# Optimization experiments

Measured on AMD Instinct MI355X. Metric: run time of the kernel, lower is better.

Reference implementation:

```python
import jax, jax.numpy as jnp
import numpy as np

LMAX = 3
L2 = (LMAX + 1) ** 2
EPS = 1e-5
N_NODES = 2048
C_IN = 384
C_HID = 256


def _gaunt_tensor(lmax):
    # Real Gaunt coefficients G[i,j,k] = integral Y_i Y_j Y_k dOmega over S^2,
    # computed exactly with Gauss-Legendre (theta) x uniform (phi) quadrature.
    nt = 4 * lmax + 4
    nph = 8 * lmax + 8
    xg, wg = np.polynomial.legendre.leggauss(nt)
    ct, st = xg, np.sqrt(1.0 - xg ** 2)
    phi = 2.0 * np.pi * np.arange(nph) / nph
    # fully-normalized associated Legendre Pbar[l,m] on theta nodes
    P = np.zeros((lmax + 1, lmax + 1, nt))
    P[0, 0] = np.sqrt(1.0 / (4.0 * np.pi))
    for m in range(1, lmax + 1):
        P[m, m] = np.sqrt((2.0 * m + 1.0) / (2.0 * m)) * st * P[m - 1, m - 1]
    for m in range(lmax + 1):
        if m + 1 <= lmax:
            P[m + 1, m] = np.sqrt(2.0 * m + 3.0) * ct * P[m, m]
        for l in range(m + 2, lmax + 1):
            a = np.sqrt((4.0 * l * l - 1.0) / (l * l - m * m))
            b = np.sqrt(((l - 1.0) ** 2 - m * m) / (4.0 * (l - 1.0) ** 2 - 1.0))
            P[l, m] = a * (ct * P[l - 1, m] - b * P[l - 2, m])
    Y = np.zeros(((lmax + 1) ** 2, nt, nph))
    for l in range(lmax + 1):
        for m in range(-l, l + 1):
            idx = l * l + l + m
            if m == 0:
                Y[idx] = P[l, 0][:, None] * np.ones((1, nph))
            elif m > 0:
                Y[idx] = np.sqrt(2.0) * P[l, m][:, None] * np.cos(m * phi)[None, :]
            else:
                Y[idx] = np.sqrt(2.0) * P[l, -m][:, None] * np.sin(-m * phi)[None, :]
    W = wg[:, None] * (2.0 * np.pi / nph)  # [nt, nph]
    G = np.einsum('iap,jap,kap->ijk', Y, Y, Y * W[None])
    G[np.abs(G) < 1e-10] = 0.0
    return G


G_NP = _gaunt_tensor(LMAX)
SL = [slice(l * l, (l + 1) * (l + 1)) for l in range(LMAX + 1)]
_raw = []
for _l1 in range(LMAX + 1):
    for _l2 in range(LMAX + 1):
        for _l3 in range(LMAX + 1):
            _blk = G_NP[SL[_l1], SL[_l2], SL[_l3]]
            if np.abs(_blk).max() > 1e-8:
                _raw.append((_l1, _l2, _l3, _blk))
_fanin = {}
for _l1, _l2, _l3, _b in _raw:
    _fanin[_l3] = _fanin.get(_l3, 0) + 1
# component irrep normalization (sqrt(2l3+1)) and path normalization (1/sqrt(fan-in))
PATHS = [(l1, l2, l3, jnp.asarray((blk * np.sqrt(2.0 * l3 + 1.0) / np.sqrt(_fanin[l3])).astype(np.float32)))
         for (l1, l2, l3, blk) in _raw]
L_OF = jnp.asarray(np.repeat(np.arange(LMAX + 1), 2 * np.arange(LMAX + 1) + 1))  # [L2]


def setup_inputs() -> dict:
    key = jax.random.key(0)
    ks = jax.random.split(key, 9)
    inputs = jax.random.normal(ks[0], (N_NODES, L2, C_IN), jnp.float32)
    batch = jnp.sort(jax.random.randint(ks[1], (N_NODES,), 0, 64))
    norm_w = 1.0 + 0.1 * jax.random.normal(ks[2], (LMAX + 1, C_IN), jnp.float32)
    norm_b = 0.02 * jax.random.normal(ks[3], (C_IN,), jnp.float32)
    w1 = jax.random.normal(ks[4], (LMAX + 1, C_IN, C_HID), jnp.float32) / np.sqrt(C_IN)
    b1 = 0.02 * jax.random.normal(ks[5], (C_HID,), jnp.float32)
    w_gaunt = jax.random.normal(ks[6], (LMAX + 1, LMAX + 1, LMAX + 1, C_HID), jnp.float32)
    w2 = jax.random.normal(ks[7], (LMAX + 1, C_HID, C_IN), jnp.float32) / np.sqrt(C_HID)
    b2 = 0.02 * jax.random.normal(ks[8], (C_IN,), jnp.float32)
    return {"inputs": inputs, "batch": batch, "norm_w": norm_w, "norm_b": norm_b,
            "w1": w1, "b1": b1, "w_gaunt": w_gaunt, "w2": w2, "b2": b2}


def _forward(inputs, norm_w, norm_b, w1, b1, w_gaunt, w2, b2):
    # equivariant merge layer norm: center l=0 over channels, RMS over all (lm, C),
    # per-degree affine weight, bias on the l=0 (invariant) component only
    x = inputs
    x = x.at[:, 0, :].add(-jnp.mean(x[:, 0, :], axis=-1, keepdims=True))
    x = x * jax.lax.rsqrt(jnp.mean(x * x, axis=(1, 2), keepdims=True) + EPS)
    x = x * norm_w[L_OF][None]          # [N, L2, C]
    x = x.at[:, 0, :].add(norm_b)
    # SO3Linear 1: per-degree channel mixing, bias on l=0
    h = jnp.einsum('nic,ich->nih', x, w1[L_OF])
    h = h.at[:, 0, :].add(b1)
    # Gaunt depthwise self tensor product: per-channel CG-structured contraction
    t = jnp.zeros((inputs.shape[0], L2, w1.shape[-1]), dtype=h.dtype)
    for (l1, l2, l3, blk) in PATHS:
        hw = h[:, SL[l2], :] * w_gaunt[l1, l2, l3][None, None, :]     # [N, 2l2+1, H]
        tmp = jnp.einsum('ijk,nih->njkh', blk, h[:, SL[l1], :])       # small block contraction
        t = t.at[:, SL[l3], :].add(jnp.einsum('njkh,njh->nkh', tmp, hw))
    # SO3Linear 2
    out = jnp.einsum('nih,iho->nio', t, w2[L_OF])
    out = out.at[:, 0, :].add(b2)
    return out + inputs  # ffn_shortcut is Identity (num_in == num_out)


def reference(inputs, batch, norm_w, norm_b, w1, b1, w_gaunt, w2, b2):
    # drop_path / proj_drop are disabled (rates = 0); `batch` only feeds GraphDropPath
    return _forward(inputs, norm_w, norm_b, w1, b1, w_gaunt, w2, b2)
```

## Files before the change

kernel.cpp:

```cpp
#include <hip/hip_runtime.h>
#include <stdint.h>
#include <math.h>
#include <array>
#include <utility>

#ifndef M_PI
#define M_PI 3.14159265358979323846
#endif

#define NNODES 2048
#define L2DIM  16
#define CIN    384
#define CHID   256

typedef __attribute__((ext_vector_type(8))) short short8;
typedef __attribute__((ext_vector_type(4))) float f32x4;
typedef unsigned short u16;
typedef unsigned int   u32;

#define LOF(i) ((i) < 1 ? 0 : ((i) < 4 ? 1 : ((i) < 9 ? 2 : 3)))

static __device__ __forceinline__ u16 f2bf(float f) {
  u32 u = __builtin_bit_cast(u32, f);
  u = u + 0x7FFFu + ((u >> 16) & 1u);
  return (u16)(u >> 16);
}
static __device__ __forceinline__ float bf2f(u16 b) {
  u32 u = ((u32)b) << 16;
  return __builtin_bit_cast(float, u);
}

constexpr double CPI = 3.14159265358979323846;

constexpr double csqrt(double x) {
  if (x <= 0.0) return 0.0;
  double y = x > 1.0 ? x : 1.0;
  for (int i = 0; i < 48; ++i) y = 0.5 * (y + x / y);
  return y;
}
constexpr double ccos(double x) {
  double r = x;
  while (r > CPI)  r -= 2.0 * CPI;
  while (r < -CPI) r += 2.0 * CPI;
  double r2 = r * r, term = 1.0, sum = 1.0;
  for (int i = 1; i <= 26; ++i) { term *= -r2 / ((2.0 * i - 1.0) * (2.0 * i)); sum += term; }
  return sum;
}
constexpr int iabs_c(int x) { return x < 0 ? -x : x; }

struct GLQ { double x[16]; double w[16]; };
constexpr GLQ build_gl() {
  GLQ g{};
  const int n = 16;
  for (int i = 0; i < n; ++i) {
    double x = ccos(CPI * (i + 0.75) / (n + 0.5));
    double p1 = 0.0, dp = 1.0;
    for (int it = 0; it < 40; ++it) {
      double p0 = 1.0; p1 = x;
      for (int k = 2; k <= n; ++k) { double p2 = ((2.0*k-1.0)*x*p1 - (k-1.0)*p0)/k; p0 = p1; p1 = p2; }
      dp = n * (x*p1 - p0) / (x*x - 1.0);
      x -= p1 / dp;
    }
    { double p0 = 1.0; p1 = x;
      for (int k = 2; k <= n; ++k) { double p2 = ((2.0*k-1.0)*x*p1 - (k-1.0)*p0)/k; p0 = p1; p1 = p2; }
      dp = n * (x*p1 - p0) / (x*x - 1.0); }
    g.x[i] = x;
    g.w[i] = 2.0 / ((1.0 - x*x) * dp * dp);
  }
  return g;
}
constexpr GLQ QG = build_gl();

struct PTab { double v[4][4][16]; };
constexpr PTab build_pbar() {
  PTab T{};
  for (int t = 0; t < 16; ++t) {
    double ct = QG.x[t];
    double st = csqrt(1.0 - ct * ct);
    double P[4][4] = {};
    P[0][0] = csqrt(1.0 / (4.0 * CPI));
    for (int m = 1; m <= 3; ++m)
      P[m][m] = csqrt((2.0*m + 1.0) / (2.0*m)) * st * P[m-1][m-1];
    for (int m = 0; m <= 3; ++m) {
      if (m + 1 <= 3) P[m+1][m] = csqrt(2.0*m + 3.0) * ct * P[m][m];
      for (int l = m + 2; l <= 3; ++l) {
        double aa = csqrt((4.0*(double)l*l - 1.0) / ((double)l*l - (double)m*m));
        double bb = csqrt(((double)(l-1)*(l-1) - (double)m*m) / (4.0*(double)(l-1)*(l-1) - 1.0));
        P[l][m] = aa * (ct * P[l-1][m] - bb * P[l-2][m]);
      }
    }
    for (int l = 0; l < 4; ++l)
      for (int m = 0; m <= l; ++m) T.v[l][m][t] = P[l][m];
  }
  return T;
}
constexpr PTab PT = build_pbar();

constexpr double phi_int(int m1, int m2, int m3) {
  const double SQ2 = 1.41421356237309504880;
  int neg = (m1 < 0) + (m2 < 0) + (m3 < 0);
  if (neg & 1) return 0.0;
  int a = iabs_c(m1), b = iabs_c(m2), c = iabs_c(m3);
  int nz = (a > 0) + (b > 0) + (c > 0);
  if (nz == 0) return 2.0 * CPI;
  if (nz == 1) return 0.0;
  if (nz == 2) {
    int p = 0, q = 0;
    if (a == 0) { p = b; q = c; } else if (b == 0) { p = a; q = c; } else { p = a; q = b; }
    return (p == q) ? 2.0 * CPI : 0.0;
  }
  if (neg == 0) {
    double v = 0.0;
    if (iabs_c(a - b) == c && a != b) v += 1.0;
    if (a + b == c) v += 1.0;
    return SQ2 * CPI * v;
  }
  int p = 0, q = 0, r = 0;
  if (m1 > 0)      { p = a; q = b; r = c; }
  else if (m2 > 0) { p = b; q = a; r = c; }
  else             { p = c; q = a; r = b; }
  double v = 0.0;
  if (q != r && p == iabs_c(q - r)) v += 1.0;
  if (p == q + r) v -= 1.0;
  return SQ2 * CPI * v;
}

constexpr bool path_ok(int l1, int l2, int l3) {
  int lo = l1 > l2 ? l1 - l2 : l2 - l1;
  return l3 >= lo && l3 <= l1 + l2 && (((l1 + l2 + l3) & 1) == 0);
}
constexpr bool term_ok(int m1, int m2, int m3) {
  int aa = iabs_c(m1), bb = iabs_c(m2), cc = iabs_c(m3);
  int neg = (m1 < 0) + (m2 < 0) + (m3 < 0);
  if (neg & 1) return false;
  return (aa + bb == cc) || (bb + cc == aa) || (cc + aa == bb);
}
constexpr int count_paths() {
  int n = 0;
  for (int l1 = 0; l1 < 4; ++l1) for (int l2 = 0; l2 < 4; ++l2) for (int l3 = 0; l3 < 4; ++l3)
    if (path_ok(l1, l2, l3)) ++n;
  return n;
}
constexpr int NPATHS = count_paths();
constexpr int NTMAX  = 512;

constexpr double term_g(int l1, int m1, int l2, int m2, int l3, int m3) {
  double ph = phi_int(m1, m2, m3);
  if (ph == 0.0) return 0.0;
  int a = iabs_c(m1), b = iabs_c(m2), c = iabs_c(m3);
  double s = 0.0;
  for (int t = 0; t < 16; ++t)
    s += QG.w[t] * PT.v[l1][a][t] * PT.v[l2][b][t] * PT.v[l3][c][t];
  double g = ph * s;
  double fan = (l3 == 0) ? 4.0 : (l3 == 1 ? 6.0 : (l3 == 2 ? 7.0 : 6.0));
  return g * csqrt((2.0 * (double)l3 + 1.0) / fan);
}

struct TermG { float g; unsigned char i, j, k, p; };
struct PathT { unsigned char l1, l2, l3; };
struct TGAll { TermG t[NTMAX]; int n; };
constexpr TGAll build_all() {
  TGAll r{};
  r.n = 0;
  int p = 0;
  for (int l1 = 0; l1 < 4; ++l1) for (int l2 = 0; l2 < 4; ++l2) for (int l3 = 0; l3 < 4; ++l3) {
    if (!path_ok(l1, l2, l3)) continue;
    for (int m1 = -l1; m1 <= l1; ++m1) for (int m2 = -l2; m2 <= l2; ++m2) for (int m3 = -l3; m3 <= l3; ++m3) {
      if (!term_ok(m1, m2, m3)) continue;
      double g = term_g(l1, m1, l2, m2, l3, m3);
      if (g > 1e-10 || g < -1e-10) {
        r.t[r.n].g = (float)g;
        r.t[r.n].i = (unsigned char)(l1 * l1 + l1 + m1);
        r.t[r.n].j = (unsigned char)(l2 * l2 + l2 + m2);
        r.t[r.n].k = (unsigned char)(l3 * l3 + l3 + m3);
        r.t[r.n].p = (unsigned char)p;
        ++r.n;
      }
    }
    ++p;
  }
  return r;
}
constexpr TGAll TGA = build_all();
constexpr int NNZ = TGA.n;

constexpr std::array<PathT, NPATHS> build_paths() {
  std::array<PathT, NPATHS> a{};
  int n = 0;
  for (int l1 = 0; l1 < 4; ++l1) for (int l2 = 0; l2 < 4; ++l2) for (int l3 = 0; l3 < 4; ++l3)
    if (path_ok(l1, l2, l3)) a[n++] = PathT{(unsigned char)l1, (unsigned char)l2, (unsigned char)l3};
  return a;
}
constexpr auto PATHS_ARR = build_paths();

template <size_t... Is>
__device__ __forceinline__ void gaunt_terms(std::index_sequence<Is...>,
    float* __restrict__ t, const float* __restrict__ h,
    const float* __restrict__ wgv) {
  ((t[TGA.t[Is].k] = fmaf(TGA.t[Is].g * wgv[TGA.t[Is].p],
                          h[TGA.t[Is].i] * h[TGA.t[Is].j],
                          t[TGA.t[Is].k])), ...);
}
template <size_t... Ps>
__device__ __forceinline__ void load_wgv2(std::index_sequence<Ps...>,
    float* __restrict__ w0, float* __restrict__ w1,
    const float* __restrict__ wg, int c) {
  float2 tmp;
  (((tmp = *reinterpret_cast<const float2*>(
        &wg[(size_t)(((int)PATHS_ARR[Ps].l1 * 4 + (int)PATHS_ARR[Ps].l2) * 4
                     + (int)PATHS_ARR[Ps].l3) * CHID + c]),
     w0[Ps] = tmp.x, w1[Ps] = tmp.y)), ...);
}

__global__ __launch_bounds__(256) void prep_kernel(
    const float* __restrict__ x, const float* __restrict__ nw,
    const float* __restrict__ nb, u16* __restrict__ xnb,
    const float* __restrict__ w1, const float* __restrict__ w2,
    u16* __restrict__ w1t, u16* __restrict__ w2t) {
  int bid = blockIdx.x, tid = threadIdx.x;
  if (bid >= NNODES) {
    __shared__ float tile[32][33];
    int b2 = bid - NNODES;
    int z = b2 / 144, rem = b2 % 144;
    int by = rem / 12, bx = rem % 12;
    int R = z < 4 ? 384 : 256, C = z < 4 ? 256 : 384;
    int r0 = by * 32, c0 = bx * 32;
    if (r0 >= R || c0 >= C) return;
    const float* s = (z < 4 ? w1 : w2) + (size_t)(z & 3) * R * C;
    u16* d = (z < 4 ? w1t : w2t) + (size_t)(z & 3) * R * C;
    int tx = tid & 31, ty = tid >> 5;
    for (int rr = ty; rr < 32; rr += 8)
      tile[rr][tx] = s[(size_t)(r0 + rr) * C + (c0 + tx)];
    __syncthreads();
    for (int cc = ty; cc < 32; cc += 8)
      d[(size_t)(c0 + cc) * R + (r0 + tx)] = f2bf(tile[tx][cc]);
    return;
  }
  int n = bid;
  const float* xr = x + (size_t)n * (L2DIM * CIN);
  __shared__ float2 red[4];
  float4 v[6];
  float ssq = 0.f, m0p = 0.f;
#pragma unroll
  for (int q = 0; q < 6; ++q) {
    v[q] = reinterpret_cast<const float4*>(xr)[tid * 6 + q];
    ssq += v[q].x*v[q].x + v[q].y*v[q].y + v[q].z*v[q].z + v[q].w*v[q].w;
  }
  if (tid < 16) {
#pragma unroll
    for (int q = 0; q < 6; ++q) m0p += v[q].x + v[q].y + v[q].z + v[q].w;
  }
  float a = m0p, b = ssq;
#pragma unroll
  for (int off = 32; off > 0; off >>= 1) { a += __shfl_down(a, off, 64); b += __shfl_down(b, off, 64); }
  int lane = tid & 63, wid = tid >> 6;
  if (lane == 0) red[wid] = make_float2(a, b);
  __syncthreads();
  float sum0 = red[0].x + red[1].x + red[2].x + red[3].x;
  float ssqt = red[0].y + red[1].y + red[2].y + red[3].y;
  float mean0 = sum0 * (1.0f / CIN);
  float ss = ssqt - (float)CIN * mean0 * mean0;
  float rstd = rsqrtf(ss * (1.0f / (L2DIM * CIN)) + 1e-5f);

  int lm = tid >> 4;
  int l = LOF(lm);
  bool row0 = (lm == 0);
  int cbase = (tid & 15) * 24;
  u16* orow = xnb + (size_t)n * (L2DIM * CIN) + (size_t)tid * 24;
#pragma unroll
  for (int q = 0; q < 6; ++q) {
    int c = cbase + q * 4;
    float4 w4 = *reinterpret_cast<const float4*>(&nw[l * CIN + c]);
    float4 b4 = row0 ? *reinterpret_cast<const float4*>(&nb[c]) : make_float4(0,0,0,0);
    float sub = row0 ? mean0 : 0.f;
    float o0 = (v[q].x - sub) * rstd * w4.x + b4.x;
    float o1 = (v[q].y - sub) * rstd * w4.y + b4.y;
    float o2 = (v[q].z - sub) * rstd * w4.z + b4.z;
    float o3 = (v[q].w - sub) * rstd * w4.w + b4.w;
    ushort4 pk;
    pk.x = f2bf(o0); pk.y = f2bf(o1); pk.z = f2bf(o2); pk.w = f2bf(o3);
    *reinterpret_cast<ushort4*>(&orow[q * 4]) = pk;
  }
}

template <int KD, int ND, int BN, bool SECOND>
__global__ __launch_bounds__(512) void so3_gemm_kernel(
    const u16* __restrict__ A, const u16* __restrict__ BT,
    const float* __restrict__ bias, const float* __restrict__ resid,
    u16* __restrict__ outb, float* __restrict__ outf) {
  constexpr int NFRAG = BN / 64;
  constexpr int WN_T = BN / 4;
  constexpr int KT = KD / 64;
  static_assert((BN % 64) == 0 && NFRAG * 16 == WN_T, "");

  int l = blockIdx.z;
  int twol1 = 2 * l + 1;
  int mtiles = (NNODES * twol1) >> 6;
  if ((int)blockIdx.x >= mtiles) return;
  int col0 = blockIdx.y * BN;
  int tid = threadIdx.x, lane = tid & 63, wid = tid >> 6;
  int wm = wid >> 2, wn = wid & 3;

  __shared__ u16 Asm[2][64 * 64];
  __shared__ u16 Bsm[2][BN * 64];

  int ar = tid >> 3;
  const u16* asrc;
  {
    int Rg = blockIdx.x * 64 + ar;
    int node = Rg / twol1;
    int lm = l * l + (Rg - node * twol1);
    asrc = A + (size_t)(node * L2DIM + lm) * KD + ((tid & 7) ^ (ar & 7)) * 8;
  }
  const u16* bsrc[BN / 64];
#pragma unroll
  for (int i = 0; i < BN / 64; ++i) {
    int r = i * 64 + (tid >> 3);
    bsrc[i] = BT + (size_t)(l * ND + col0 + r) * KD + ((tid & 7) ^ (r & 7)) * 8;
  }

  auto stage = [&](int buf, int kt) {
    __builtin_amdgcn_global_load_lds(
        (const __attribute__((address_space(1))) void*)(asrc + kt * 64),
        (__attribute__((address_space(3))) void*)(&Asm[buf][wid * 512]),
        16, 0, 0);
#pragma unroll
    for (int i = 0; i < BN / 64; ++i)
      __builtin_amdgcn_global_load_lds(
          (const __attribute__((address_space(1))) void*)(bsrc[i] + kt * 64),
          (__attribute__((address_space(3))) void*)(&Bsm[buf][i * 4096 + wid * 512]),
          16, 0, 0);
  };

  f32x4 acc[2][NFRAG];
#pragma unroll
  for (int i = 0; i < 2; ++i)
#pragma unroll
    for (int j = 0; j < NFRAG; ++j) acc[i][j] = (f32x4){0.f, 0.f, 0.f, 0.f};

  stage(0, 0);
  __syncthreads();
#pragma unroll
  for (int kt = 0; kt < KT; ++kt) {
    int cur = kt & 1;
    if (kt + 1 < KT) stage(cur ^ 1, kt + 1);
#pragma unroll
    for (int ks = 0; ks < 2; ++ks) {
      short8 af[2], bfv[NFRAG];
#pragma unroll
      for (int mf = 0; mf < 2; ++mf) {
        int row = wm * 32 + mf * 16 + (lane & 15);
        int slot = (ks * 4 + (lane >> 4)) ^ (row & 7);
        af[mf] = *reinterpret_cast<const short8*>(&Asm[cur][row * 64 + slot * 8]);
      }
#pragma unroll
      for (int nf = 0; nf < NFRAG; ++nf) {
        int brow = wn * WN_T + nf * 16 + (lane & 15);
        int slot = (ks * 4 + (lane >> 4)) ^ (brow & 7);
        bfv[nf] = *reinterpret_cast<const short8*>(&Bsm[cur][brow * 64 + slot * 8]);
      }
#pragma unroll
      for (int mf = 0; mf < 2; ++mf)
#pragma unroll
        for (int nf = 0; nf < NFRAG; ++nf)
          acc[mf][nf] = __builtin_amdgcn_mfma_f32_16x16x32_bf16(af[mf], bfv[nf], acc[mf][nf], 0, 0, 0);
    }
    __syncthreads();
  }

#pragma unroll
  for (int mf = 0; mf < 2; ++mf) {
#pragma unroll
    for (int jj = 0; jj < 4; ++jj) {
      int Rg = blockIdx.x * 64 + wm * 32 + mf * 16 + (lane >> 4) * 4 + jj;
      int node = Rg / twol1;
      int lm = l * l + (Rg - node * twol1);
      size_t rowoff = (size_t)(node * L2DIM + lm);
#pragma unroll
      for (int nf = 0; nf < NFRAG; ++nf) {
        int colg = col0 + wn * WN_T + nf * 16 + (lane & 15);
        float vv = acc[mf][nf][jj];
        if (l == 0) vv += bias[colg];
        if (!SECOND) {
          outb[rowoff * ND + colg] = f2bf(vv);
        } else {
          outf[rowoff * ND + colg] = vv + resid[rowoff * ND + colg];
        }
      }
    }
  }
}

__global__ __launch_bounds__(256) void gaunt_kernel(
    const u16* __restrict__ hb, const float* __restrict__ wg,
    u16* __restrict__ tb) {
  int tid = threadIdx.x;
  int n = blockIdx.x * 2 + (tid >> 7);
  int c = (tid & 127) * 2;
  const u16* hr = hb + (size_t)n * (L2DIM * CHID) + c;
  float h0[16], h1[16];
#pragma unroll
  for (int i = 0; i < 16; ++i) {
    u32 w = *reinterpret_cast<const u32*>(&hr[i * CHID]);
    h0[i] = bf2f((u16)(w & 0xffffu));
    h1[i] = bf2f((u16)(w >> 16));
  }

  float w0[NPATHS], w1[NPATHS];
  load_wgv2(std::make_index_sequence<NPATHS>{}, w0, w1, wg, c);

  float t0[16], t1[16];
#pragma unroll
  for (int k = 0; k < 16; ++k) { t0[k] = 0.f; t1[k] = 0.f; }

  gaunt_terms(std::make_index_sequence<NNZ>{}, t0, h0, w0);
  gaunt_terms(std::make_index_sequence<NNZ>{}, t1, h1, w1);

  u16* tr = tb + (size_t)n * (L2DIM * CHID) + c;
#pragma unroll
  for (int k = 0; k < 16; ++k) {
    u32 o = (u32)f2bf(t0[k]) | ((u32)f2bf(t1[k]) << 16);
    *reinterpret_cast<u32*>(&tr[k * CHID]) = o;
  }
}

extern "C" void kernel_launch(void* const* d_in, const int* in_sizes, int n_in,
                              void* d_out, int out_size, void* d_ws, size_t ws_size,
                              hipStream_t stream) {
  const float* inputs = (const float*)d_in[0];
  const float* norm_w = (const float*)d_in[2];
  const float* norm_b = (const float*)d_in[3];
  const float* w1     = (const float*)d_in[4];
  const float* b1     = (const float*)d_in[5];
  const float* wga    = (const float*)d_in[6];
  const float* w2     = (const float*)d_in[7];
  const float* b2     = (const float*)d_in[8];
  float* out = (float*)d_out;

  uint8_t* ws = (uint8_t*)d_ws;
  u16*   w1t = (u16*)(ws + 16384);
  u16*   w2t = (u16*)(ws + 802816);
  u16*   xnb = (u16*)(ws + 1589248);
  u16*   tb  = xnb;
  u16*   hb  = (u16*)(ws + 26755072);

  prep_kernel<<<NNODES + 1152, 256, 0, stream>>>(
      inputs, norm_w, norm_b, xnb, w1, w2, w1t, w2t);
  so3_gemm_kernel<CIN, CHID, 128, false><<<dim3(224, 2, 4), 512, 0, stream>>>(
      xnb, w1t, b1, nullptr, hb, nullptr);
  gaunt_kernel<<<NNODES / 2, 256, 0, stream>>>(hb, wga, tb);
  so3_gemm_kernel<CHID, CIN, 128, true><<<dim3(224, 3, 4), 512, 0, stream>>>(
      tb, w2t, b2, inputs, nullptr, out);
}
```

Baseline: 83.60 us.

## Swap GEMM operand roles so each lane writes contiguous channel vectors

The SO3 linear GEMMs are recast in transposed form. Weights now fill the MFMA A side with 64 channels per block, and node rows fill the B side with 128 rows per block. In the epilogue each lane then holds four consecutive output channels, so bias, residual and output can be moved with vectorized float4/ushort4 accesses instead of scalar strided stores. The grid shape changes to match the new 128x64 tile, which changes how much of each operand is reused per block and the total block count.

```diff
diff --git a/kernel.cpp b/kernel.cpp
--- a/kernel.cpp
+++ b/kernel.cpp
@@ -283,60 +283,53 @@
   }
 }
 
-template <int KD, int ND, int BN, bool SECOND>
+template <int KD, int NDC, bool SECOND>
 __global__ __launch_bounds__(512) void so3_gemm_kernel(
-    const u16* __restrict__ A, const u16* __restrict__ BT,
+    const u16* __restrict__ X, const u16* __restrict__ WT,
     const float* __restrict__ bias, const float* __restrict__ resid,
     u16* __restrict__ outb, float* __restrict__ outf) {
-  constexpr int NFRAG = BN / 64;
-  constexpr int WN_T = BN / 4;
   constexpr int KT = KD / 64;
-  static_assert((BN % 64) == 0 && NFRAG * 16 == WN_T, "");
-
   int l = blockIdx.z;
   int twol1 = 2 * l + 1;
-  int mtiles = (NNODES * twol1) >> 6;
-  if ((int)blockIdx.x >= mtiles) return;
-  int col0 = blockIdx.y * BN;
+  if ((int)blockIdx.x >= 16 * twol1) return;
+  int bx = blockIdx.x, by = blockIdx.y;
   int tid = threadIdx.x, lane = tid & 63, wid = tid >> 6;
   int wm = wid >> 2, wn = wid & 3;
 
-  __shared__ u16 Asm[2][64 * 64];
-  __shared__ u16 Bsm[2][BN * 64];
-
-  int ar = tid >> 3;
-  const u16* asrc;
-  {
-    int Rg = blockIdx.x * 64 + ar;
+  __shared__ u16 Wsm[2][64 * 64];
+  __shared__ u16 Xsm[2][128 * 64];
+
+  int wr = tid >> 3;
+  const u16* wsrc = WT + (size_t)(l * NDC + by * 64 + wr) * KD
+                       + ((tid & 7) ^ (wr & 7)) * 8;
+  const u16* xsrc[2];
+#pragma unroll
+  for (int i = 0; i < 2; ++i) {
+    int xr = i * 64 + (tid >> 3);
+    int Rg = bx * 128 + xr;
     int node = Rg / twol1;
     int lm = l * l + (Rg - node * twol1);
-    asrc = A + (size_t)(node * L2DIM + lm) * KD + ((tid & 7) ^ (ar & 7)) * 8;
-  }
-  const u16* bsrc[BN / 64];
-#pragma unroll
-  for (int i = 0; i < BN / 64; ++i) {
-    int r = i * 64 + (tid >> 3);
-    bsrc[i] = BT + (size_t)(l * ND + col0 + r) * KD + ((tid & 7) ^ (r & 7)) * 8;
+    xsrc[i] = X + (size_t)(node * L2DIM + lm) * KD + ((tid & 7) ^ (xr & 7)) * 8;
   }
 
   auto stage = [&](int buf, int kt) {
     __builtin_amdgcn_global_load_lds(
-        (const __attribute__((address_space(1))) void*)(asrc + kt * 64),
-        (__attribute__((address_space(3))) void*)(&Asm[buf][wid * 512]),
+        (const __attribute__((address_space(1))) void*)(wsrc + kt * 64),
+        (__attribute__((address_space(3))) void*)(&Wsm[buf][wid * 512]),
         16, 0, 0);
 #pragma unroll
-    for (int i = 0; i < BN / 64; ++i)
+    for (int i = 0; i < 2; ++i)
       __builtin_amdgcn_global_load_lds(
-          (const __attribute__((address_space(1))) void*)(bsrc[i] + kt * 64),
-          (__attribute__((address_space(3))) void*)(&Bsm[buf][i * 4096 + wid * 512]),
+          (const __attribute__((address_space(1))) void*)(xsrc[i] + kt * 64),
+          (__attribute__((address_space(3))) void*)(&Xsm[buf][i * 4096 + wid * 512]),
           16, 0, 0);
   };
 
-  f32x4 acc[2][NFRAG];
+  f32x4 acc[2][2];
 #pragma unroll
   for (int i = 0; i < 2; ++i)
 #pragma unroll
-    for (int j = 0; j < NFRAG; ++j) acc[i][j] = (f32x4){0.f, 0.f, 0.f, 0.f};
+    for (int j = 0; j < 2; ++j) acc[i][j] = (f32x4){0.f, 0.f, 0.f, 0.f};
 
   stage(0, 0);
   __syncthreads();
@@ -346,24 +339,24 @@
     if (kt + 1 < KT) stage(cur ^ 1, kt + 1);
 #pragma unroll
     for (int ks = 0; ks < 2; ++ks) {
-      short8 af[2], bfv[NFRAG];
+      short8 wf[2], xf[2];
 #pragma unroll
       for (int mf = 0; mf < 2; ++mf) {
         int row = wm * 32 + mf * 16 + (lane & 15);
         int slot = (ks * 4 + (lane >> 4)) ^ (row & 7);
-        af[mf] = *reinterpret_cast<const short8*>(&Asm[cur][row * 64 + slot * 8]);
-      }
-#pragma unroll
-      for (int nf = 0; nf < NFRAG; ++nf) {
-        int brow = wn * WN_T + nf * 16 + (lane & 15);
-        int slot = (ks * 4 + (lane >> 4)) ^ (brow & 7);
-        bfv[nf] = *reinterpret_cast<const short8*>(&Bsm[cur][brow * 64 + slot * 8]);
+        wf[mf] = *reinterpret_cast<const short8*>(&Wsm[cur][row * 64 + slot * 8]);
+      }
+#pragma unroll
+      for (int nf = 0; nf < 2; ++nf) {
+        int row = wn * 32 + nf * 16 + (lane & 15);
+        int slot = (ks * 4 + (lane >> 4)) ^ (row & 7);
+        xf[nf] = *reinterpret_cast<const short8*>(&Xsm[cur][row * 64 + slot * 8]);
       }
 #pragma unroll
       for (int mf = 0; mf < 2; ++mf)
 #pragma unroll
-        for (int nf = 0; nf < NFRAG; ++nf)
-          acc[mf][nf] = __builtin_amdgcn_mfma_f32_16x16x32_bf16(af[mf], bfv[nf], acc[mf][nf], 0, 0, 0);
+        for (int nf = 0; nf < 2; ++nf)
+          acc[mf][nf] = __builtin_amdgcn_mfma_f32_16x16x32_bf16(wf[mf], xf[nf], acc[mf][nf], 0, 0, 0);
     }
     __syncthreads();
   }
@@ -371,21 +364,26 @@
 #pragma unroll
   for (int mf = 0; mf < 2; ++mf) {
 #pragma unroll
-    for (int jj = 0; jj < 4; ++jj) {
-      int Rg = blockIdx.x * 64 + wm * 32 + mf * 16 + (lane >> 4) * 4 + jj;
-      int node = Rg / twol1;
-      int lm = l * l + (Rg - node * twol1);
-      size_t rowoff = (size_t)(node * L2DIM + lm);
-#pragma unroll
-      for (int nf = 0; nf < NFRAG; ++nf) {
-        int colg = col0 + wn * WN_T + nf * 16 + (lane & 15);
-        float vv = acc[mf][nf][jj];
-        if (l == 0) vv += bias[colg];
-        if (!SECOND) {
-          outb[rowoff * ND + colg] = f2bf(vv);
-        } else {
-          outf[rowoff * ND + colg] = vv + resid[rowoff * ND + colg];
-        }
+    for (int nf = 0; nf < 2; ++nf) {
+      int nodelm_g = bx * 128 + wn * 32 + nf * 16 + (lane & 15);
+      int node = nodelm_g / twol1;
+      int lm = l * l + (nodelm_g - node * twol1);
+      int chan0 = by * 64 + wm * 32 + mf * 16 + (lane >> 4) * 4;
+      size_t base = (size_t)(node * L2DIM + lm) * NDC + chan0;
+      float4 v = make_float4(acc[mf][nf][0], acc[mf][nf][1],
+                             acc[mf][nf][2], acc[mf][nf][3]);
+      if (l == 0) {
+        float4 b4 = *reinterpret_cast<const float4*>(&bias[chan0]);
+        v.x += b4.x; v.y += b4.y; v.z += b4.z; v.w += b4.w;
+      }
+      if (!SECOND) {
+        ushort4 pk;
+        pk.x = f2bf(v.x); pk.y = f2bf(v.y); pk.z = f2bf(v.z); pk.w = f2bf(v.w);
+        *reinterpret_cast<ushort4*>(&outb[base]) = pk;
+      } else {
+        float4 rv = *reinterpret_cast<const float4*>(&resid[base]);
+        v.x += rv.x; v.y += rv.y; v.z += rv.z; v.w += rv.w;
+        *reinterpret_cast<float4*>(&outf[base]) = v;
       }
     }
   }
@@ -446,9 +444,9 @@
 
   prep_kernel<<<NNODES + 1152, 256, 0, stream>>>(
       inputs, norm_w, norm_b, xnb, w1, w2, w1t, w2t);
-  so3_gemm_kernel<CIN, CHID, 128, false><<<dim3(224, 2, 4), 512, 0, stream>>>(
+  so3_gemm_kernel<CIN, CHID, false><<<dim3(112, 4, 4), 512, 0, stream>>>(
       xnb, w1t, b1, nullptr, hb, nullptr);
   gaunt_kernel<<<NNODES / 2, 256, 0, stream>>>(hb, wga, tb);
-  so3_gemm_kernel<CHID, CIN, 128, true><<<dim3(224, 3, 4), 512, 0, stream>>>(
+  so3_gemm_kernel<CHID, CIN, true><<<dim3(112, 6, 4), 512, 0, stream>>>(
       tb, w2t, b2, inputs, nullptr, out);
 }
```

New measurement: 87.40 us. 4.5% more time.
